# Optimization experiments

Hardware: AMD Instinct MI355X
Metric: run time of the kernel (lower is better)

Reference implementation:

```python
import jax, jax.numpy as jnp
import numpy as np

B, M, N, C = 8192, 16, 256, 64


def setup_inputs() -> dict:
    key = jax.random.key(0)
    k1, k2 = jax.random.split(key)
    inputs = jax.random.normal(k1, (B, M, C), dtype=jnp.float32)
    codebook = jax.random.normal(k2, (M, N, C), dtype=jnp.float32)
    return {"inputs": inputs, "codebook": codebook}


def reference(inputs, codebook):
    # inputs: [B, M, C]; codebook: [M, N, C]
    # (avoids materializing the torch [B, M, N, C] broadcast difference)
    x2 = jnp.sum(inputs * inputs, axis=-1)[:, :, None]          # [B, M, 1]
    c2 = jnp.sum(codebook * codebook, axis=-1)[None, :, :]      # [1, M, N]
    xc = jnp.einsum('bmc,mnc->bmn', inputs, codebook)           # [B, M, N]
    dist = x2 - 2.0 * xc + c2                                   # [B, M, N]
    idx = jnp.argmin(dist, axis=-1)                             # [B, M] int
    m_idx = jnp.arange(codebook.shape[0])[None, :]              # [1, M]
    codes = codebook[m_idx, idx]                                # [B, M, C]
    return codes, idx
```

## Files before the change

### kernel.cpp

```cpp
#include <hip/hip_runtime.h>
#include <hip/hip_bf16.h>
#include <float.h>


#define BQ 8192
#define MQ 16
#define NQ 256
#define CQ 64
#define RPB 128
#define XP 72

typedef short  shortx8 __attribute__((ext_vector_type(8)));
typedef float  f32x4   __attribute__((ext_vector_type(4)));

__device__ __forceinline__ unsigned short f2bf(float f, float& rem) {
    __hip_bfloat16 h = __float2bfloat16(f);
    rem = f - __bfloat162float(h);
    return __builtin_bit_cast(unsigned short, h);
}

__global__ __launch_bounds__(256) void fq_prep_kernel(
        const float* __restrict__ codebook,
        unsigned short* __restrict__ cb3,
        float* __restrict__ c2) {
    const int e = blockIdx.x * 256 + threadIdx.x;
    const int m = e >> 8, n = e & 255;
    const float* row = codebook + (size_t)e * CQ;

    float s = 0.0f;
    #pragma unroll
    for (int kc = 0; kc < CQ; kc += 8) {
        const float4 va = *(const float4*)(row + kc);
        const float4 vb = *(const float4*)(row + kc + 4);
        const float el[8] = {va.x, va.y, va.z, va.w, vb.x, vb.y, vb.z, vb.w};
        uint p0[4], p1[4], p2[4];
        #pragma unroll
        for (int u = 0; u < 4; ++u) {
            float r;
            const float a = el[2 * u], b = el[2 * u + 1];
            s = fmaf(a, a, fmaf(b, b, s));
            const unsigned short a0 = f2bf(a, r);  float ra = r;
            const unsigned short a1 = f2bf(ra, r); float ra2 = r;
            float dummy;
            const unsigned short a2 = f2bf(ra2, dummy);
            const unsigned short b0 = f2bf(b, r);  float rb = r;
            const unsigned short b1 = f2bf(rb, r); float rb2 = r;
            const unsigned short b2 = f2bf(rb2, dummy);
            p0[u] = (uint)a0 | ((uint)b0 << 16);
            p1[u] = (uint)a1 | ((uint)b1 << 16);
            p2[u] = (uint)a2 | ((uint)b2 << 16);
        }
        #pragma unroll
        for (int sp = 0; sp < 3; ++sp) {
            const uint* p = (sp == 0) ? p0 : (sp == 1) ? p1 : p2;
            uint4* dst = (uint4*)(cb3 + (((size_t)m * 3 + sp) * NQ + n) * CQ + kc);
            *dst = make_uint4(p[0], p[1], p[2], p[3]);
        }
    }
    c2[e] = s;
}

__global__ __launch_bounds__(256, 2) void fq_main_kernel(
        const float* __restrict__ inputs,
        const float* __restrict__ codebook,
        const unsigned short* __restrict__ cb3,
        const float* __restrict__ c2,
        float* __restrict__ out_codes,
        float* __restrict__ out_idx) {
    const int m    = blockIdx.y;
    const int row0 = blockIdx.x * RPB;
    const int w    = threadIdx.x >> 6;
    const int lane = threadIdx.x & 63;
    const int quad = lane >> 4;
    const int col  = lane & 15;
    const int wrow = w * 32;

    __shared__ unsigned short sx[3][RPB][XP];
    __shared__ unsigned short sb[RPB][XP];
    __shared__ float s_c2[NQ];
    __shared__ int   s_bi[RPB];

    s_c2[threadIdx.x] = c2[m * NQ + threadIdx.x];

    {
        const int r = threadIdx.x >> 1, hh = threadIdx.x & 1;
        const float* xp = inputs + ((size_t)(row0 + r) * MQ + m) * CQ + hh * 32;
        #pragma unroll
        for (int kc = 0; kc < 32; kc += 8) {
            const float4 va = *(const float4*)(xp + kc);
            const float4 vb = *(const float4*)(xp + kc + 4);
            const float el[8] = {va.x, va.y, va.z, va.w, vb.x, vb.y, vb.z, vb.w};
            uint p0[4], p1[4], p2[4];
            #pragma unroll
            for (int u = 0; u < 4; ++u) {
                float r1, r2, dummy;
                const float a = el[2 * u], b = el[2 * u + 1];
                const unsigned short a0 = f2bf(a, r1);
                const unsigned short a1 = f2bf(r1, r2);
                const unsigned short a2 = f2bf(r2, dummy);
                const unsigned short b0 = f2bf(b, r1);
                const unsigned short b1 = f2bf(r1, r2);
                const unsigned short b2 = f2bf(r2, dummy);
                p0[u] = (uint)a0 | ((uint)b0 << 16);
                p1[u] = (uint)a1 | ((uint)b1 << 16);
                p2[u] = (uint)a2 | ((uint)b2 << 16);
            }
            uint* d0 = (uint*)&sx[0][r][hh * 32 + kc];
            uint* d1 = (uint*)&sx[1][r][hh * 32 + kc];
            uint* d2 = (uint*)&sx[2][r][hh * 32 + kc];
            #pragma unroll
            for (int u = 0; u < 4; ++u) { d0[u] = p0[u]; d1[u] = p1[u]; d2[u] = p2[u]; }
        }
    }

    f32x4 acc[2][16];
    #pragma unroll
    for (int rt = 0; rt < 2; ++rt)
        #pragma unroll
        for (int nt = 0; nt < 16; ++nt)
            acc[rt][nt] = (f32x4){0.f, 0.f, 0.f, 0.f};

    #pragma unroll
    for (int ch = 0; ch < 2; ++ch) {
        #pragma unroll
        for (int j = 0; j < 3; ++j) {
            __syncthreads();
            {
                const int n = threadIdx.x >> 1, hh = threadIdx.x & 1;
                const uint4* src = (const uint4*)(
                    cb3 + (((size_t)m * 3 + j) * NQ + ch * 128 + n) * CQ + hh * 32);
                uint4* dst = (uint4*)&sb[n][hh * 32];
                #pragma unroll
                for (int q = 0; q < 4; ++q) dst[q] = src[q];
            }
            __syncthreads();

            #pragma unroll
            for (int h = 0; h < 2; ++h) {
                shortx8 bf[8];
                #pragma unroll
                for (int ntl = 0; ntl < 8; ++ntl)
                    bf[ntl] = *(const shortx8*)&sb[ntl * 16 + col][h * 32 + quad * 8];
                #pragma unroll
                for (int i = 0; i <= 2 - j; ++i) {
                    const shortx8 a0 = *(const shortx8*)&sx[i][wrow + col][h * 32 + quad * 8];
                    const shortx8 a1 = *(const shortx8*)&sx[i][wrow + 16 + col][h * 32 + quad * 8];
                    #pragma unroll
                    for (int ntl = 0; ntl < 8; ++ntl) {
                        acc[0][ch * 8 + ntl] = __builtin_amdgcn_mfma_f32_16x16x32_bf16(
                            a0, bf[ntl], acc[0][ch * 8 + ntl], 0, 0, 0);
                        acc[1][ch * 8 + ntl] = __builtin_amdgcn_mfma_f32_16x16x32_bf16(
                            a1, bf[ntl], acc[1][ch * 8 + ntl], 0, 0, 0);
                    }
                }
            }
        }
    }

    float c2r[16];
    #pragma unroll
    for (int nt = 0; nt < 16; ++nt) c2r[nt] = s_c2[nt * 16 + col];

    #pragma unroll
    for (int rt = 0; rt < 2; ++rt) {
        #pragma unroll
        for (int reg = 0; reg < 4; ++reg) {
            float bd = FLT_MAX; int bi = 0;
            #pragma unroll
            for (int nt = 0; nt < 16; ++nt) {
                const float d = fmaf(-2.0f, acc[rt][nt][reg], c2r[nt]);
                if (d < bd) { bd = d; bi = nt * 16 + col; }
            }
            #pragma unroll
            for (int mask = 1; mask <= 8; mask <<= 1) {
                const float od = __shfl_xor(bd, mask, 64);
                const int   oi = __shfl_xor(bi, mask, 64);
                if (od < bd || (od == bd && oi < bi)) { bd = od; bi = oi; }
            }
            if (col == 0)
                s_bi[wrow + rt * 16 + quad * 4 + reg] = bi;
        }
    }
    __syncthreads();

    if (threadIdx.x < RPB)
        out_idx[(size_t)(row0 + threadIdx.x) * MQ + m] = (float)s_bi[threadIdx.x];

    const float* cbm = codebook + (size_t)m * NQ * CQ;
    #pragma unroll 4
    for (int jj = 0; jj < 32; ++jj) {
        const int r  = w * 32 + jj;
        const int bn = s_bi[r];
        out_codes[((size_t)(row0 + r) * MQ + m) * CQ + lane] =
            cbm[(size_t)bn * CQ + lane];
    }
}

extern "C" void kernel_launch(void* const* d_in, const int* in_sizes, int n_in,
                              void* d_out, int out_size, void* d_ws, size_t ws_size,
                              hipStream_t stream) {
    const float* inputs   = (const float*)d_in[0];
    const float* codebook = (const float*)d_in[1];
    float* out_codes = (float*)d_out;
    float* out_idx   = (float*)d_out + (size_t)BQ * MQ * CQ;
    float*          c2  = (float*)d_ws;
    unsigned short* cb3 = (unsigned short*)(c2 + MQ * NQ);

    fq_prep_kernel<<<dim3(MQ * NQ / 256), 256, 0, stream>>>(codebook, cb3, c2);

    fq_main_kernel<<<dim3(BQ / RPB, MQ), 256, 0, stream>>>(
        inputs, codebook, cb3, c2, out_codes, out_idx);
}
```

Baseline: 123.2 us.

## Pre-swizzle codebook into MFMA fragment layout and split codewords across waves

The prep kernel now uses eight threads per codeword and writes the three-way bf16 split of the codebook directly in MFMA B-fragment order, so the main kernel loads B fragments straight from global memory with no LDS staging or barriers. The main kernel handles 64 rows per block instead of 128. Each wave owns 32 rows and half of the codewords, and the two halves' argmin results are merged through shared memory. Input splitting now happens in registers from an fp32 LDS tile, and occupancy is raised to three blocks per CU. The cost is more global traffic for B fragments, twice as many blocks, and an extra cross-wave reduction step.

```diff
diff --git a/kernel.cpp b/kernel.cpp
--- a/kernel.cpp
+++ b/kernel.cpp
@@ -7,8 +7,6 @@
 #define MQ 16
 #define NQ 256
 #define CQ 64
-#define RPB 128
-#define XP 72
 
 typedef short  shortx8 __attribute__((ext_vector_type(8)));
 typedef float  f32x4   __attribute__((ext_vector_type(4)));
@@ -21,145 +19,143 @@
 
 __global__ __launch_bounds__(256) void fq_prep_kernel(
         const float* __restrict__ codebook,
-        unsigned short* __restrict__ cb3,
+        unsigned short* __restrict__ cb3f,
         float* __restrict__ c2) {
-    const int e = blockIdx.x * 256 + threadIdx.x;
-    const int m = e >> 8, n = e & 255;
-    const float* row = codebook + (size_t)e * CQ;
+    const int t  = blockIdx.x * 256 + threadIdx.x;
+    const int kc = t & 7;
+    const int e  = t >> 3;
+    const int m  = e >> 8, n = e & 255;
+    const int nt = n >> 4, col = n & 15;
+    const int h = kc >> 2, quad = kc & 3;
+
+    const float* src = codebook + (size_t)e * CQ + kc * 8;
+    const float4 va = *(const float4*)src;
+    const float4 vb = *(const float4*)(src + 4);
+    const float el[8] = {va.x, va.y, va.z, va.w, vb.x, vb.y, vb.z, vb.w};
 
     float s = 0.0f;
     #pragma unroll
-    for (int kc = 0; kc < CQ; kc += 8) {
-        const float4 va = *(const float4*)(row + kc);
-        const float4 vb = *(const float4*)(row + kc + 4);
-        const float el[8] = {va.x, va.y, va.z, va.w, vb.x, vb.y, vb.z, vb.w};
-        uint p0[4], p1[4], p2[4];
-        #pragma unroll
-        for (int u = 0; u < 4; ++u) {
-            float r;
-            const float a = el[2 * u], b = el[2 * u + 1];
-            s = fmaf(a, a, fmaf(b, b, s));
-            const unsigned short a0 = f2bf(a, r);  float ra = r;
-            const unsigned short a1 = f2bf(ra, r); float ra2 = r;
-            float dummy;
-            const unsigned short a2 = f2bf(ra2, dummy);
-            const unsigned short b0 = f2bf(b, r);  float rb = r;
-            const unsigned short b1 = f2bf(rb, r); float rb2 = r;
-            const unsigned short b2 = f2bf(rb2, dummy);
-            p0[u] = (uint)a0 | ((uint)b0 << 16);
-            p1[u] = (uint)a1 | ((uint)b1 << 16);
-            p2[u] = (uint)a2 | ((uint)b2 << 16);
-        }
-        #pragma unroll
-        for (int sp = 0; sp < 3; ++sp) {
-            const uint* p = (sp == 0) ? p0 : (sp == 1) ? p1 : p2;
-            uint4* dst = (uint4*)(cb3 + (((size_t)m * 3 + sp) * NQ + n) * CQ + kc);
-            *dst = make_uint4(p[0], p[1], p[2], p[3]);
-        }
-    }
-    c2[e] = s;
-}
-
-__global__ __launch_bounds__(256, 2) void fq_main_kernel(
+    for (int u = 0; u < 8; ++u) s = fmaf(el[u], el[u], s);
+    s += __shfl_xor(s, 1, 64);
+    s += __shfl_xor(s, 2, 64);
+    s += __shfl_xor(s, 4, 64);
+    if (kc == 0) c2[e] = s;
+
+    uint p0[4], p1[4], p2[4];
+    #pragma unroll
+    for (int u = 0; u < 4; ++u) {
+        float r1, r2, d;
+        const float a = el[2 * u], b = el[2 * u + 1];
+        const unsigned short a0 = f2bf(a, r1);
+        const unsigned short a1 = f2bf(r1, r2);
+        const unsigned short a2 = f2bf(r2, d);
+        const unsigned short b0 = f2bf(b, r1);
+        const unsigned short b1 = f2bf(r1, r2);
+        const unsigned short b2 = f2bf(r2, d);
+        p0[u] = (uint)a0 | ((uint)b0 << 16);
+        p1[u] = (uint)a1 | ((uint)b1 << 16);
+        p2[u] = (uint)a2 | ((uint)b2 << 16);
+    }
+    const int lane_f = quad * 16 + col;
+    #pragma unroll
+    for (int j = 0; j < 3; ++j) {
+        const uint* p = (j == 0) ? p0 : (j == 1) ? p1 : p2;
+        const int frag = ((m * 3 + j) * 2 + h) * 16 + nt;
+        uint4* dst = (uint4*)(cb3f + ((size_t)frag * 64 + lane_f) * 8);
+        *dst = make_uint4(p[0], p[1], p[2], p[3]);
+    }
+}
+
+__global__ __launch_bounds__(256, 3) void fq_main_kernel(
         const float* __restrict__ inputs,
         const float* __restrict__ codebook,
-        const unsigned short* __restrict__ cb3,
+        const unsigned short* __restrict__ cb3f,
         const float* __restrict__ c2,
         float* __restrict__ out_codes,
         float* __restrict__ out_idx) {
     const int m    = blockIdx.y;
-    const int row0 = blockIdx.x * RPB;
+    const int row0 = blockIdx.x * 64;
     const int w    = threadIdx.x >> 6;
     const int lane = threadIdx.x & 63;
     const int quad = lane >> 4;
     const int col  = lane & 15;
-    const int wrow = w * 32;
-
-    __shared__ unsigned short sx[3][RPB][XP];
-    __shared__ unsigned short sb[RPB][XP];
+    const int rg   = w & 1;
+    const int chh  = w >> 1;
+
+    __shared__ float sxf[64][68];
     __shared__ float s_c2[NQ];
-    __shared__ int   s_bi[RPB];
+    __shared__ float s_wb[2][64];
+    __shared__ int   s_wi[2][64];
+    __shared__ int   s_win[64];
 
     s_c2[threadIdx.x] = c2[m * NQ + threadIdx.x];
 
-    {
-        const int r = threadIdx.x >> 1, hh = threadIdx.x & 1;
-        const float* xp = inputs + ((size_t)(row0 + r) * MQ + m) * CQ + hh * 32;
-        #pragma unroll
-        for (int kc = 0; kc < 32; kc += 8) {
-            const float4 va = *(const float4*)(xp + kc);
-            const float4 vb = *(const float4*)(xp + kc + 4);
+    #pragma unroll
+    for (int i = 0; i < 4; ++i) {
+        const int f = threadIdx.x + 256 * i;
+        const int r = f >> 4;
+        const int c = (f & 15) * 4;
+        const float4 v = *(const float4*)(
+            inputs + ((size_t)(row0 + r) * MQ + m) * CQ + c);
+        *(float4*)&sxf[r][c] = v;
+    }
+    __syncthreads();
+
+    shortx8 afr[3][2][2];
+    #pragma unroll
+    for (int rt = 0; rt < 2; ++rt)
+        #pragma unroll
+        for (int h = 0; h < 2; ++h) {
+            const float* xp = &sxf[rg * 32 + rt * 16 + col][h * 32 + quad * 8];
+            const float4 va = *(const float4*)xp;
+            const float4 vb = *(const float4*)(xp + 4);
             const float el[8] = {va.x, va.y, va.z, va.w, vb.x, vb.y, vb.z, vb.w};
-            uint p0[4], p1[4], p2[4];
-            #pragma unroll
-            for (int u = 0; u < 4; ++u) {
-                float r1, r2, dummy;
-                const float a = el[2 * u], b = el[2 * u + 1];
-                const unsigned short a0 = f2bf(a, r1);
-                const unsigned short a1 = f2bf(r1, r2);
-                const unsigned short a2 = f2bf(r2, dummy);
-                const unsigned short b0 = f2bf(b, r1);
-                const unsigned short b1 = f2bf(r1, r2);
-                const unsigned short b2 = f2bf(r2, dummy);
-                p0[u] = (uint)a0 | ((uint)b0 << 16);
-                p1[u] = (uint)a1 | ((uint)b1 << 16);
-                p2[u] = (uint)a2 | ((uint)b2 << 16);
-            }
-            uint* d0 = (uint*)&sx[0][r][hh * 32 + kc];
-            uint* d1 = (uint*)&sx[1][r][hh * 32 + kc];
-            uint* d2 = (uint*)&sx[2][r][hh * 32 + kc];
-            #pragma unroll
-            for (int u = 0; u < 4; ++u) { d0[u] = p0[u]; d1[u] = p1[u]; d2[u] = p2[u]; }
+            shortx8 a0, a1, a2;
+            #pragma unroll
+            for (int u = 0; u < 8; ++u) {
+                float r1, r2, d;
+                a0[u] = (short)f2bf(el[u], r1);
+                a1[u] = (short)f2bf(r1, r2);
+                a2[u] = (short)f2bf(r2, d);
+            }
+            afr[0][rt][h] = a0; afr[1][rt][h] = a1; afr[2][rt][h] = a2;
         }
-    }
-
-    f32x4 acc[2][16];
+
+    f32x4 acc[2][8];
     #pragma unroll
     for (int rt = 0; rt < 2; ++rt)
         #pragma unroll
-        for (int nt = 0; nt < 16; ++nt)
+        for (int nt = 0; nt < 8; ++nt)
             acc[rt][nt] = (f32x4){0.f, 0.f, 0.f, 0.f};
 
     #pragma unroll
-    for (int ch = 0; ch < 2; ++ch) {
+    for (int h = 0; h < 2; ++h) {
         #pragma unroll
         for (int j = 0; j < 3; ++j) {
-            __syncthreads();
-            {
-                const int n = threadIdx.x >> 1, hh = threadIdx.x & 1;
-                const uint4* src = (const uint4*)(
-                    cb3 + (((size_t)m * 3 + j) * NQ + ch * 128 + n) * CQ + hh * 32);
-                uint4* dst = (uint4*)&sb[n][hh * 32];
+            const int frag0 = ((m * 3 + j) * 2 + h) * 16 + chh * 8;
+            const unsigned short* bp =
+                cb3f + ((size_t)frag0 * 64 + lane) * 8;
+            shortx8 bfr[8];
+            #pragma unroll
+            for (int nt = 0; nt < 8; ++nt)
+                bfr[nt] = *(const shortx8*)(bp + (size_t)nt * 64 * 8);
+            #pragma unroll
+            for (int i = 0; i <= 2 - j; ++i) {
                 #pragma unroll
-                for (int q = 0; q < 4; ++q) dst[q] = src[q];
-            }
-            __syncthreads();
-
-            #pragma unroll
-            for (int h = 0; h < 2; ++h) {
-                shortx8 bf[8];
-                #pragma unroll
-                for (int ntl = 0; ntl < 8; ++ntl)
-                    bf[ntl] = *(const shortx8*)&sb[ntl * 16 + col][h * 32 + quad * 8];
-                #pragma unroll
-                for (int i = 0; i <= 2 - j; ++i) {
-                    const shortx8 a0 = *(const shortx8*)&sx[i][wrow + col][h * 32 + quad * 8];
-                    const shortx8 a1 = *(const shortx8*)&sx[i][wrow + 16 + col][h * 32 + quad * 8];
-                    #pragma unroll
-                    for (int ntl = 0; ntl < 8; ++ntl) {
-                        acc[0][ch * 8 + ntl] = __builtin_amdgcn_mfma_f32_16x16x32_bf16(
-                            a0, bf[ntl], acc[0][ch * 8 + ntl], 0, 0, 0);
-                        acc[1][ch * 8 + ntl] = __builtin_amdgcn_mfma_f32_16x16x32_bf16(
-                            a1, bf[ntl], acc[1][ch * 8 + ntl], 0, 0, 0);
-                    }
+                for (int nt = 0; nt < 8; ++nt) {
+                    acc[0][nt] = __builtin_amdgcn_mfma_f32_16x16x32_bf16(
+                        afr[i][0][h], bfr[nt], acc[0][nt], 0, 0, 0);
+                    acc[1][nt] = __builtin_amdgcn_mfma_f32_16x16x32_bf16(
+                        afr[i][1][h], bfr[nt], acc[1][nt], 0, 0, 0);
                 }
             }
         }
     }
 
-    float c2r[16];
-    #pragma unroll
-    for (int nt = 0; nt < 16; ++nt) c2r[nt] = s_c2[nt * 16 + col];
+    float c2r[8];
+    #pragma unroll
+    for (int nt = 0; nt < 8; ++nt)
+        c2r[nt] = s_c2[chh * 128 + nt * 16 + col];
 
     #pragma unroll
     for (int rt = 0; rt < 2; ++rt) {
@@ -167,9 +163,9 @@
         for (int reg = 0; reg < 4; ++reg) {
             float bd = FLT_MAX; int bi = 0;
             #pragma unroll
-            for (int nt = 0; nt < 16; ++nt) {
+            for (int nt = 0; nt < 8; ++nt) {
                 const float d = fmaf(-2.0f, acc[rt][nt][reg], c2r[nt]);
-                if (d < bd) { bd = d; bi = nt * 16 + col; }
+                if (d < bd) { bd = d; bi = chh * 128 + nt * 16 + col; }
             }
             #pragma unroll
             for (int mask = 1; mask <= 8; mask <<= 1) {
@@ -177,20 +173,29 @@
                 const int   oi = __shfl_xor(bi, mask, 64);
                 if (od < bd || (od == bd && oi < bi)) { bd = od; bi = oi; }
             }
-            if (col == 0)
-                s_bi[wrow + rt * 16 + quad * 4 + reg] = bi;
+            if (col == 0) {
+                const int r = rg * 32 + rt * 16 + quad * 4 + reg;
+                s_wb[chh][r] = bd;
+                s_wi[chh][r] = bi;
+            }
         }
     }
     __syncthreads();
 
-    if (threadIdx.x < RPB)
-        out_idx[(size_t)(row0 + threadIdx.x) * MQ + m] = (float)s_bi[threadIdx.x];
+    if (w == 0) {
+        float bd = s_wb[0][lane]; int bi = s_wi[0][lane];
+        const float od = s_wb[1][lane]; const int oi = s_wi[1][lane];
+        if (od < bd || (od == bd && oi < bi)) { bd = od; bi = oi; }
+        s_win[lane] = bi;
+        out_idx[(size_t)(row0 + lane) * MQ + m] = (float)bi;
+    }
+    __syncthreads();
 
     const float* cbm = codebook + (size_t)m * NQ * CQ;
     #pragma unroll 4
-    for (int jj = 0; jj < 32; ++jj) {
-        const int r  = w * 32 + jj;
-        const int bn = s_bi[r];
+    for (int jj = 0; jj < 16; ++jj) {
+        const int r  = w * 16 + jj;
+        const int bn = s_win[r];
         out_codes[((size_t)(row0 + r) * MQ + m) * CQ + lane] =
             cbm[(size_t)bn * CQ + lane];
     }
@@ -203,11 +208,11 @@
     const float* codebook = (const float*)d_in[1];
     float* out_codes = (float*)d_out;
     float* out_idx   = (float*)d_out + (size_t)BQ * MQ * CQ;
-    float*          c2  = (float*)d_ws;
-    unsigned short* cb3 = (unsigned short*)(c2 + MQ * NQ);
-
-    fq_prep_kernel<<<dim3(MQ * NQ / 256), 256, 0, stream>>>(codebook, cb3, c2);
-
-    fq_main_kernel<<<dim3(BQ / RPB, MQ), 256, 0, stream>>>(
-        inputs, codebook, cb3, c2, out_codes, out_idx);
-}
+    float*          c2   = (float*)d_ws;
+    unsigned short* cb3f = (unsigned short*)(c2 + MQ * NQ);
+
+    fq_prep_kernel<<<dim3(128), 256, 0, stream>>>(codebook, cb3f, c2);
+
+    fq_main_kernel<<<dim3(BQ / 64, MQ), 256, 0, stream>>>(
+        inputs, codebook, cb3f, c2, out_codes, out_idx);
+}
```

Result: faster. 120.7 us (-2.1%).
